# Kernel tuning notes

Measured on AMD Instinct MI355X. Metric: run time of the kernel, lower is better.

Reference implementation:

```python
import jax, jax.numpy as jnp
import numpy as np

WINDOW_SIZE = 11
NUM_BINS = 256
SIGMA = 1.5
C1 = 0.01 ** 2
C2 = 0.03 ** 2
MAX_PSNR = 40.0


def _gaussian_window():
    xs = jnp.arange(WINDOW_SIZE, dtype=jnp.float32)
    g = jnp.exp(-((xs - WINDOW_SIZE // 2) ** 2) / (2.0 * SIGMA ** 2))
    g = g / g.sum()
    w2 = jnp.outer(g, g)  # [11,11]
    return jnp.broadcast_to(w2[None, None], (3, 1, WINDOW_SIZE, WINDOW_SIZE))


def setup_inputs() -> dict:
    key = jax.random.key(0)
    k1, k2 = jax.random.split(key)
    B, C, H, W = 64, 3, 256, 256
    x = jax.random.uniform(k1, (B, C, H, W), dtype=jnp.float32) * 2.0 - 1.0
    y = jax.random.uniform(k2, (B, C, H, W), dtype=jnp.float32) * 2.0 - 1.0
    return {"x": x, "y": y, "window": _gaussian_window()}


def _depthwise_conv(img, w):
    pad = WINDOW_SIZE // 2
    return jax.lax.conv_general_dilated(
        img, w, window_strides=(1, 1), padding=[(pad, pad), (pad, pad)],
        feature_group_count=img.shape[1],
        dimension_numbers=("NCHW", "OIHW", "NCHW"))


def _mi(x, y):
    B = x.shape[0]
    nb = NUM_BINS
    xf = (x.reshape(B, -1) + 1.0) * 0.5  # [B, N] in [0,1]
    yf = (y.reshape(B, -1) + 1.0) * 0.5
    N = xf.shape[1]
    ix = jnp.clip((xf * nb).astype(jnp.int32), 0, nb - 1)
    iy = jnp.clip((yf * nb).astype(jnp.int32), 0, nb - 1)
    flat = (jnp.arange(B, dtype=jnp.int32)[:, None] * (nb * nb) + ix * nb + iy).reshape(-1)
    hist = jnp.zeros(B * nb * nb, jnp.float32).at[flat].add(1.0).reshape(B, nb, nb)
    jp = hist / N  # joint probs [B, nb, nb]
    px = jp.sum(axis=2)  # [B, nb]
    py = jp.sum(axis=1)

    def ent(p):
        return -jnp.sum(jnp.where(p > 0, p * jnp.log2(jnp.where(p > 0, p, 1.0)), 0.0), axis=-1)

    hx = ent(px)
    hy = ent(py)
    pxy = px[:, :, None] * py[:, None, :]
    ratio = jp / jnp.where(pxy > 0, pxy, 1.0)
    mi = jnp.sum(jnp.where(jp > 0, jp * jnp.log2(jnp.where(jp > 0, ratio, 1.0)), 0.0), axis=(1, 2))
    norm = jnp.minimum(hx, hy)  # mi_method='min'
    mi = jnp.where(norm > 0, mi / norm, 0.0)
    return jnp.clip(mi, 0.0, 1.0)


def _ssim(x, y, window):
    mu1 = _depthwise_conv(x, window)
    mu2 = _depthwise_conv(y, window)
    mu1_sq = mu1 * mu1
    mu2_sq = mu2 * mu2
    mu1_mu2 = mu1 * mu2
    sigma1_sq = _depthwise_conv(x * x, window) - mu1_sq
    sigma2_sq = _depthwise_conv(y * y, window) - mu2_sq
    sigma12 = _depthwise_conv(x * y, window) - mu1_mu2
    ssim_map = ((2 * mu1_mu2 + C1) * (2 * sigma12 + C2)) / ((mu1_sq + mu2_sq + C1) * (sigma1_sq + sigma2_sq + C2))
    return ssim_map.mean(axis=(1, 2, 3))


def _psnr(x, y):
    xr = x * 0.5 + 0.5
    yr = y * 0.5 + 0.5
    mse = jnp.mean((xr - yr) ** 2, axis=(1, 2, 3))
    zero = mse == 0
    mse = jnp.where(zero, 1e-8, mse)
    psnr = -10.0 * jnp.log10(mse)  # 20*log10(1.0) == 0
    return jnp.where(zero, 100.0, psnr) / MAX_PSNR


def reference(x, y, window):
    mi_vals = _mi(x, y)
    ssim_vals = _ssim(x, y, window)
    psnr_vals = _psnr(x, y)
    metrics = jnp.stack([mi_vals, ssim_vals, psnr_vals], axis=1)  # [B,3]
    return metrics[:, :, None]  # [B,3,1]
```

## Files before the change

### kernel.cpp

```cpp
#include <hip/hip_runtime.h>
#include <cstdint>
#include <cstddef>

#define BATCH 64
#define CH 3
#define HH 256
#define WW 256
#define NBINS 256
#define TILE 32
#define HALO 5
#define NPB (CH*HH*WW)
#define QPX (NPB/4)
#define NHB 256

__device__ __forceinline__ float block_reduce_256(float v, float* buf4) {
    #pragma unroll
    for (int o = 32; o > 0; o >>= 1) v += __shfl_down(v, o, 64);
    __syncthreads();
    int lane = threadIdx.x & 63;
    int wid  = threadIdx.x >> 6;
    if (lane == 0) buf4[wid] = v;
    __syncthreads();
    return buf4[0] + buf4[1] + buf4[2] + buf4[3];
}

__device__ __forceinline__ float block_reduce_1024(float v, float* buf16) {
    #pragma unroll
    for (int o = 32; o > 0; o >>= 1) v += __shfl_down(v, o, 64);
    __syncthreads();
    int lane = threadIdx.x & 63;
    int wid  = threadIdx.x >> 6;
    if (lane == 0) buf16[wid] = v;
    __syncthreads();
    float s = 0.0f;
    #pragma unroll
    for (int i = 0; i < 16; i++) s += buf16[i];
    return s;
}

__global__ __launch_bounds__(256) void mega_kernel(
    const float* __restrict__ x, const float* __restrict__ y,
    const float* __restrict__ win,
    float* __restrict__ ssim_partials,
    unsigned int* __restrict__ u4hist, float* __restrict__ mse_part)
{
    __shared__ __align__(16) unsigned char smem[32768];
    const int bid = blockIdx.x;
    const int tid = threadIdx.x;

    if (bid < NHB) {
        unsigned int* h32 = (unsigned int*)smem;
        uint4* h128 = (uint4*)h32;
        #pragma unroll
        for (int i = 0; i < 8; i++) h128[tid + i * 256] = make_uint4(0, 0, 0, 0);
        __syncthreads();

        const int b = bid >> 2, e = bid & 3;
        const float4* x4 = (const float4*)x + (size_t)b * (NPB/4) + (size_t)e * (QPX/4);
        const float4* y4 = (const float4*)y + (size_t)b * (NPB/4) + (size_t)e * (QPX/4);
        float mse_s = 0.0f;
        for (int i = 0; i < 48; i++) {
            float4 xv = x4[tid + i * 256];
            float4 yv = y4[tid + i * 256];
            float xs[4] = {xv.x, xv.y, xv.z, xv.w};
            float ys[4] = {yv.x, yv.y, yv.z, yv.w};
            #pragma unroll
            for (int q = 0; q < 4; q++) {
                float xc = xs[q], yc = ys[q];
                float d = xc - yc;
                mse_s += d * d;
                int ix = (int)(((xc + 1.0f) * 0.5f) * 256.0f);
                int iy = (int)(((yc + 1.0f) * 0.5f) * 256.0f);
                ix = min(max(ix, 0), 255);
                iy = min(max(iy, 0), 255);
                int key = ix * NBINS + iy;
                atomicAdd(&h32[key >> 3], 1u << (4 * (key & 7)));
            }
        }
        #pragma unroll
        for (int o = 32; o > 0; o >>= 1) mse_s += __shfl_down(mse_s, o, 64);
        if ((tid & 63) == 0) mse_part[bid * 4 + (tid >> 6)] = mse_s;
        __syncthreads();

        #pragma unroll
        for (int k = 0; k < 32; k++)
            u4hist[(size_t)bid * 8192 + tid + k * 256] = h32[tid + k * 256];
        return;
    }

    typedef float4 (*hA4_t)[33];
    hA4_t hA4 = (hA4_t)smem;
    float* g    = (float*)(smem + 22176);
    float* rbuf = (float*)(smem + 22240);

    const int cb = bid - NHB;
    const int tx = cb & 7, ty = (cb >> 3) & 7, z = cb >> 6;
    const float* xi = x + (size_t)z * (HH * WW);
    const float* yi = y + (size_t)z * (HH * WW);

    if (tid < 11) {
        float g5 = sqrtf(win[5*11 + 5]);
        g[tid] = win[5*11 + tid] / g5;
    }
    __syncthreads();

    if (tid < 42 * 4) {
        int r = tid >> 2;
        int c0 = (tid & 3) * 8;
        int gr = ty * TILE - HALO + r;
        int gw = tx * TILE + c0 - HALO;
        float xw[18], yw[18];
        bool rowok = (gr >= 0 && gr < HH);
        if (rowok) {
            const float* xr = xi + gr * WW;
            const float* yr = yi + gr * WW;
            int ga = gw - 3;
            if (ga >= 0 && ga + 24 <= WW) {
                float t0[24], t1[24];
                const float4* px4 = (const float4*)(xr + ga);
                const float4* py4 = (const float4*)(yr + ga);
                #pragma unroll
                for (int q = 0; q < 6; q++) {
                    float4 a = px4[q], bb = py4[q];
                    t0[q*4+0]=a.x; t0[q*4+1]=a.y; t0[q*4+2]=a.z; t0[q*4+3]=a.w;
                    t1[q*4+0]=bb.x; t1[q*4+1]=bb.y; t1[q*4+2]=bb.z; t1[q*4+3]=bb.w;
                }
                #pragma unroll
                for (int i = 0; i < 18; i++) { xw[i] = t0[3+i]; yw[i] = t1[3+i]; }
            } else {
                #pragma unroll
                for (int i = 0; i < 18; i++) {
                    int gc = gw + i;
                    bool ok = (gc >= 0 && gc < WW);
                    xw[i] = ok ? xr[gc] : 0.0f;
                    yw[i] = ok ? yr[gc] : 0.0f;
                }
            }
        } else {
            #pragma unroll
            for (int i = 0; i < 18; i++) { xw[i] = 0.0f; yw[i] = 0.0f; }
        }

        float aX[8], aY[8], aU[8], aV[8];
        #pragma unroll
        for (int j = 0; j < 8; j++) { aX[j]=0; aY[j]=0; aU[j]=0; aV[j]=0; }
        #pragma unroll
        for (int i = 0; i < 18; i++) {
            float xv = xw[i], yv = yw[i];
            float uu = xv * xv + yv * yv;
            float vv = xv * yv;
            #pragma unroll
            for (int j = 0; j < 8; j++) {
                int k = i - j;
                if (k >= 0 && k < 11) {
                    float w = g[k];
                    aX[j] += w * xv;
                    aY[j] += w * yv;
                    aU[j] += w * uu;
                    aV[j] += w * vv;
                }
            }
        }
        #pragma unroll
        for (int j = 0; j < 8; j++)
            hA4[r][c0 + j] = make_float4(aX[j], aY[j], aU[j], aV[j]);
    }
    __syncthreads();

    const int c  = tid & 31;
    const int r0 = (tid >> 5) * 4;
    float mu1[4], mu2[4], euv[4], exy[4];
    #pragma unroll
    for (int j = 0; j < 4; j++) { mu1[j]=0; mu2[j]=0; euv[j]=0; exy[j]=0; }
    #pragma unroll
    for (int i = 0; i < 14; i++) {
        float4 v = hA4[r0 + i][c];
        #pragma unroll
        for (int j = 0; j < 4; j++) {
            int k = i - j;
            if (k >= 0 && k < 11) {
                float w = g[k];
                mu1[j] += w * v.x;
                mu2[j] += w * v.y;
                euv[j] += w * v.z;
                exy[j] += w * v.w;
            }
        }
    }

    float ssim_s = 0.0f;
    const float C1v = 1e-4f, C2v = 9e-4f;
    #pragma unroll
    for (int j = 0; j < 4; j++) {
        float m1 = mu1[j], m2 = mu2[j];
        float m1s = m1 * m1, m2s = m2 * m2, m12 = m1 * m2;
        float ssum = euv[j] - m1s - m2s;
        float s12  = exy[j] - m12;
        float num = (2.0f * m12 + C1v) * (2.0f * s12 + C2v);
        float den = (m1s + m2s + C1v) * (ssum + C2v);
        ssim_s += num / den;
    }

    float ssim_b = block_reduce_256(ssim_s, rbuf);
    if (tid == 0)
        ssim_partials[(size_t)z * 64 + ty * 8 + tx] = ssim_b;
}

__global__ __launch_bounds__(1024) void merge_finalize_kernel(
    const unsigned int* __restrict__ u4hist,
    const float* __restrict__ mse_part, const float* __restrict__ ssim_partials,
    float* __restrict__ out)
{
    __shared__ unsigned int colw[16][256];
    __shared__ float rbuf[16];
    const int b = blockIdx.x, t = threadIdx.x;
    const int w = t >> 6, l = t & 63;
    const float invN = 1.0f / (float)NPB;

    #pragma unroll
    for (int i = 0; i < 4; i++) ((unsigned int*)colw)[t + i * 1024] = 0;
    __syncthreads();

    float sxy = 0.0f, sx = 0.0f;
    for (int s = 0; s < 4; s++) {
        unsigned int s0a = 0, s1a = 0, s0b = 0, s1b = 0;
        #pragma unroll
        for (int p = 0; p < 4; p++) {
            const uint2* src = (const uint2*)(u4hist + (size_t)(b * 4 + p) * 8192 + s * 2048);
            uint2 v = src[t];
            s0a += v.x & 0x0F0F0F0Fu;  s1a += (v.x >> 4) & 0x0F0F0F0Fu;
            s0b += v.y & 0x0F0F0F0Fu;  s1b += (v.y >> 4) & 0x0F0F0F0Fu;
        }
        unsigned int cnt[16];
        #pragma unroll
        for (int m = 0; m < 4; m++) {
            cnt[2*m]         = (s0a >> (8*m)) & 255u;
            cnt[2*m + 1]     = (s1a >> (8*m)) & 255u;
            cnt[8 + 2*m]     = (s0b >> (8*m)) & 255u;
            cnt[8 + 2*m + 1] = (s1b >> (8*m)) & 255u;
        }

        unsigned int rowc = 0;
        #pragma unroll
        for (int k = 0; k < 16; k++) {
            unsigned int v = cnt[k];
            rowc += v;
            if (v) {
                float jp = (float)v * invN;
                sxy += jp * __log2f(jp);
            }
        }
        #pragma unroll
        for (int o = 8; o > 0; o >>= 1) rowc += __shfl_xor((int)rowc, o, 16);
        if ((t & 15) == 0 && rowc) {
            float px = (float)rowc * invN;
            sx += px * __log2f(px);
        }

        #pragma unroll
        for (int k = 0; k < 16; k++) {
            cnt[k] += __shfl_xor((int)cnt[k], 16, 64);
            cnt[k] += __shfl_xor((int)cnt[k], 32, 64);
        }
        if (l < 16) {
            #pragma unroll
            for (int k = 0; k < 16; k++) colw[w][16 * l + k] += cnt[k];
        }
    }

    float sxy_blk = block_reduce_1024(sxy, rbuf);
    float sx_blk  = block_reduce_1024(sx, rbuf);

    float ey = 0.0f;
    if (t < 256) {
        unsigned int pc = 0;
        #pragma unroll
        for (int ww = 0; ww < 16; ww++) pc += colw[ww][t];
        if (pc) {
            float py = (float)pc * invN;
            ey = -py * __log2f(py);
        }
    }
    float hy = block_reduce_1024(ey, rbuf);
    float ssim_total = block_reduce_1024(
        (t < 192) ? ssim_partials[(size_t)b * 192 + t] : 0.0f, rbuf);
    float mse_all = block_reduce_1024(
        (t < 16) ? mse_part[b * 16 + t] : 0.0f, rbuf);

    if (t == 0) {
        float hxy = -sxy_blk;
        float hx  = -sx_blk;
        float mi = hx + hy - hxy;
        float norm = fminf(hx, hy);
        float m = (norm > 0.0f) ? (mi / norm) : 0.0f;
        m = fminf(fmaxf(m, 0.0f), 1.0f);
        out[b * 3 + 0] = m;
        out[b * 3 + 1] = ssim_total * invN;
        double mse = (double)mse_all * (1.0 / (4.0 * (double)NPB));
        out[b * 3 + 2] = (mse == 0.0) ? 2.5f : (float)(-10.0 * log10(mse) / 40.0);
    }
}

extern "C" void kernel_launch(void* const* d_in, const int* in_sizes, int n_in,
                              void* d_out, int out_size, void* d_ws, size_t ws_size,
                              hipStream_t stream) {
    const float* x   = (const float*)d_in[0];
    const float* y   = (const float*)d_in[1];
    const float* win = (const float*)d_in[2];
    float* out = (float*)d_out;

    char* p = (char*)d_ws;
    unsigned int* u4hist = (unsigned int*)p;
    size_t off = (size_t)NHB * 8192 * sizeof(unsigned int);
    float* mse_part = (float*)(p + off);        off += (size_t)NHB * 4 * sizeof(float);
    float* ssim_partials = (float*)(p + off);

    mega_kernel<<<dim3(NHB + 8 * 8 * BATCH * CH), dim3(256), 0, stream>>>(
        x, y, win, ssim_partials, u4hist, mse_part);
    merge_finalize_kernel<<<dim3(BATCH), dim3(1024), 0, stream>>>(
        u4hist, mse_part, ssim_partials, out);
}
```

Measured before the change: 183.7 us.

## Replace 2D tiled SSIM with per-column streaming row sweep over bands

The SSIM blocks now each own one 32-row band of a full 256-wide image plane. Each thread owns one column and sweeps 42 rows. A row is double-buffered through per-wave shared memory, the horizontal 11-tap pass is computed per row, and the vertical pass uses an 11-deep register sliding accumulator. This cuts halo recomputation from 2D tiles and removes the large shared tile plus its block-wide barriers, and it lowers the SSIM block count. The cost is a serial 42-iteration loop per thread with scalar loads, a heavier register footprint under the new launch-bounds occupancy hint, fewer blocks for the GPU to schedule, and a fast approximate divide.

```diff
diff --git a/kernel.cpp b/kernel.cpp
--- a/kernel.cpp
+++ b/kernel.cpp
@@ -7,11 +7,12 @@
 #define HH 256
 #define WW 256
 #define NBINS 256
-#define TILE 32
-#define HALO 5
 #define NPB (CH*HH*WW)
 #define QPX (NPB/4)
 #define NHB 256
+#define NZ (BATCH*CH)
+#define NBANDS 8
+#define NCB (NZ*NBANDS)
 
 __device__ __forceinline__ float block_reduce_256(float v, float* buf4) {
     #pragma unroll
@@ -38,7 +39,7 @@
     return s;
 }
 
-__global__ __launch_bounds__(256) void mega_kernel(
+__global__ __launch_bounds__(256, 5) void mega_kernel(
     const float* __restrict__ x, const float* __restrict__ y,
     const float* __restrict__ win,
     float* __restrict__ ssim_partials,
@@ -88,122 +89,114 @@
         return;
     }
 
-    typedef float4 (*hA4_t)[33];
-    hA4_t hA4 = (hA4_t)smem;
-    float* g    = (float*)(smem + 22176);
-    float* rbuf = (float*)(smem + 22240);
+    float* wbuf = (float*)smem;
+    float* rbuf = (float*)(smem + 5120);
 
     const int cb = bid - NHB;
-    const int tx = cb & 7, ty = (cb >> 3) & 7, z = cb >> 6;
+    const int z = cb >> 3, band = cb & 7;
+    const int w = tid >> 6, l = tid & 63;
+    float* wb = wbuf + w * 320;
+
     const float* xi = x + (size_t)z * (HH * WW);
     const float* yi = y + (size_t)z * (HH * WW);
 
-    if (tid < 11) {
-        float g5 = sqrtf(win[5*11 + 5]);
-        g[tid] = win[5*11 + tid] / g5;
-    }
-    __syncthreads();
-
-    if (tid < 42 * 4) {
-        int r = tid >> 2;
-        int c0 = (tid & 3) * 8;
-        int gr = ty * TILE - HALO + r;
-        int gw = tx * TILE + c0 - HALO;
-        float xw[18], yw[18];
-        bool rowok = (gr >= 0 && gr < HH);
-        if (rowok) {
+    float gw[11];
+    {
+        float gs = sqrtf(win[60]);
+        #pragma unroll
+        for (int k = 0; k < 11; k++) gw[k] = win[55 + k] / gs;
+    }
+
+    const int r0g = band * 32 - 5;
+    const int gc  = tid - 5;
+    const int gc2 = gc + 64;
+    const bool okc  = (gc >= 0);
+    const bool okc2 = (gc2 < WW);
+
+    float aX[11], aY[11], aU[11], aV[11];
+    #pragma unroll
+    for (int j = 0; j < 11; j++) { aX[j]=0.0f; aY[j]=0.0f; aU[j]=0.0f; aV[j]=0.0f; }
+
+    {
+        int gr = r0g;
+        bool okr = (gr >= 0) && (gr < HH);
+        const float* xr = xi + gr * WW;
+        const float* yr = yi + gr * WW;
+        float xv = (okr && okc) ? xr[gc] : 0.0f;
+        float yv = (okr && okc) ? yr[gc] : 0.0f;
+        wb[l]      = xv;
+        wb[80 + l] = yv;
+        if (l < 10) {
+            float xv2 = (okr && okc2) ? xr[gc2] : 0.0f;
+            float yv2 = (okr && okc2) ? yr[gc2] : 0.0f;
+            wb[l + 64]      = xv2;
+            wb[80 + l + 64] = yv2;
+        }
+    }
+
+    float ssim_s = 0.0f;
+    const float C1v = 1e-4f, C2v = 9e-4f;
+    #pragma unroll 1
+    for (int r = 0; r < 42; ++r) {
+        const int p = r & 1;
+        float* cur = wb + p * 160;
+        if (r < 41) {
+            int gr = r0g + r + 1;
+            bool okr = (gr >= 0) && (gr < HH);
             const float* xr = xi + gr * WW;
             const float* yr = yi + gr * WW;
-            int ga = gw - 3;
-            if (ga >= 0 && ga + 24 <= WW) {
-                float t0[24], t1[24];
-                const float4* px4 = (const float4*)(xr + ga);
-                const float4* py4 = (const float4*)(yr + ga);
-                #pragma unroll
-                for (int q = 0; q < 6; q++) {
-                    float4 a = px4[q], bb = py4[q];
-                    t0[q*4+0]=a.x; t0[q*4+1]=a.y; t0[q*4+2]=a.z; t0[q*4+3]=a.w;
-                    t1[q*4+0]=bb.x; t1[q*4+1]=bb.y; t1[q*4+2]=bb.z; t1[q*4+3]=bb.w;
-                }
-                #pragma unroll
-                for (int i = 0; i < 18; i++) { xw[i] = t0[3+i]; yw[i] = t1[3+i]; }
-            } else {
-                #pragma unroll
-                for (int i = 0; i < 18; i++) {
-                    int gc = gw + i;
-                    bool ok = (gc >= 0 && gc < WW);
-                    xw[i] = ok ? xr[gc] : 0.0f;
-                    yw[i] = ok ? yr[gc] : 0.0f;
-                }
+            float xv = (okr && okc) ? xr[gc] : 0.0f;
+            float yv = (okr && okc) ? yr[gc] : 0.0f;
+            float* nxt = wb + (p ^ 1) * 160;
+            nxt[l]      = xv;
+            nxt[80 + l] = yv;
+            if (l < 10) {
+                float xv2 = (okr && okc2) ? xr[gc2] : 0.0f;
+                float yv2 = (okr && okc2) ? yr[gc2] : 0.0f;
+                nxt[l + 64]      = xv2;
+                nxt[80 + l + 64] = yv2;
             }
-        } else {
-            #pragma unroll
-            for (int i = 0; i < 18; i++) { xw[i] = 0.0f; yw[i] = 0.0f; }
-        }
-
-        float aX[8], aY[8], aU[8], aV[8];
-        #pragma unroll
-        for (int j = 0; j < 8; j++) { aX[j]=0; aY[j]=0; aU[j]=0; aV[j]=0; }
-        #pragma unroll
-        for (int i = 0; i < 18; i++) {
-            float xv = xw[i], yv = yw[i];
-            float uu = xv * xv + yv * yv;
-            float vv = xv * yv;
-            #pragma unroll
-            for (int j = 0; j < 8; j++) {
-                int k = i - j;
-                if (k >= 0 && k < 11) {
-                    float w = g[k];
-                    aX[j] += w * xv;
-                    aY[j] += w * yv;
-                    aU[j] += w * uu;
-                    aV[j] += w * vv;
-                }
-            }
-        }
-        #pragma unroll
-        for (int j = 0; j < 8; j++)
-            hA4[r][c0 + j] = make_float4(aX[j], aY[j], aU[j], aV[j]);
-    }
-    __syncthreads();
-
-    const int c  = tid & 31;
-    const int r0 = (tid >> 5) * 4;
-    float mu1[4], mu2[4], euv[4], exy[4];
-    #pragma unroll
-    for (int j = 0; j < 4; j++) { mu1[j]=0; mu2[j]=0; euv[j]=0; exy[j]=0; }
-    #pragma unroll
-    for (int i = 0; i < 14; i++) {
-        float4 v = hA4[r0 + i][c];
-        #pragma unroll
-        for (int j = 0; j < 4; j++) {
-            int k = i - j;
-            if (k >= 0 && k < 11) {
-                float w = g[k];
-                mu1[j] += w * v.x;
-                mu2[j] += w * v.y;
-                euv[j] += w * v.z;
-                exy[j] += w * v.w;
-            }
-        }
-    }
-
-    float ssim_s = 0.0f;
-    const float C1v = 1e-4f, C2v = 9e-4f;
-    #pragma unroll
-    for (int j = 0; j < 4; j++) {
-        float m1 = mu1[j], m2 = mu2[j];
-        float m1s = m1 * m1, m2s = m2 * m2, m12 = m1 * m2;
-        float ssum = euv[j] - m1s - m2s;
-        float s12  = exy[j] - m12;
-        float num = (2.0f * m12 + C1v) * (2.0f * s12 + C2v);
-        float den = (m1s + m2s + C1v) * (ssum + C2v);
-        ssim_s += num / den;
+        }
+        float hx = 0.0f, hy = 0.0f, hu = 0.0f, hv = 0.0f;
+        #pragma unroll
+        for (int k = 0; k < 11; ++k) {
+            float a  = cur[l + k];
+            float b2 = cur[80 + l + k];
+            float wk = gw[k];
+            hx = fmaf(wk, a, hx);
+            hy = fmaf(wk, b2, hy);
+            float uu = fmaf(b2, b2, a * a);
+            hu = fmaf(wk, uu, hu);
+            float vv = a * b2;
+            hv = fmaf(wk, vv, hv);
+        }
+        #pragma unroll
+        for (int j = 0; j < 11; ++j) {
+            float wj = gw[10 - j];
+            aX[j] = fmaf(wj, hx, aX[j]);
+            aY[j] = fmaf(wj, hy, aY[j]);
+            aU[j] = fmaf(wj, hu, aU[j]);
+            aV[j] = fmaf(wj, hv, aV[j]);
+        }
+        if (r >= 10) {
+            float m1 = aX[0], m2 = aY[0];
+            float m1s = m1 * m1, m2s = m2 * m2, m12 = m1 * m2;
+            float ssum = aU[0] - m1s - m2s;
+            float s12  = aV[0] - m12;
+            float num = (2.0f * m12 + C1v) * (2.0f * s12 + C2v);
+            float den = (m1s + m2s + C1v) * (ssum + C2v);
+            ssim_s += __fdividef(num, den);
+        }
+        #pragma unroll
+        for (int j = 0; j < 10; ++j) {
+            aX[j] = aX[j+1]; aY[j] = aY[j+1]; aU[j] = aU[j+1]; aV[j] = aV[j+1];
+        }
+        aX[10] = 0.0f; aY[10] = 0.0f; aU[10] = 0.0f; aV[10] = 0.0f;
     }
 
     float ssim_b = block_reduce_256(ssim_s, rbuf);
     if (tid == 0)
-        ssim_partials[(size_t)z * 64 + ty * 8 + tx] = ssim_b;
+        ssim_partials[(size_t)z * NBANDS + band] = ssim_b;
 }
 
 __global__ __launch_bounds__(1024) void merge_finalize_kernel(
@@ -283,7 +276,7 @@
     }
     float hy = block_reduce_1024(ey, rbuf);
     float ssim_total = block_reduce_1024(
-        (t < 192) ? ssim_partials[(size_t)b * 192 + t] : 0.0f, rbuf);
+        (t < 24) ? ssim_partials[(size_t)b * 24 + t] : 0.0f, rbuf);
     float mse_all = block_reduce_1024(
         (t < 16) ? mse_part[b * 16 + t] : 0.0f, rbuf);
 
@@ -315,7 +308,7 @@
     float* mse_part = (float*)(p + off);        off += (size_t)NHB * 4 * sizeof(float);
     float* ssim_partials = (float*)(p + off);
 
-    mega_kernel<<<dim3(NHB + 8 * 8 * BATCH * CH), dim3(256), 0, stream>>>(
+    mega_kernel<<<dim3(NHB + NCB), dim3(256), 0, stream>>>(
         x, y, win, ssim_partials, u4hist, mse_part);
     merge_finalize_kernel<<<dim3(BATCH), dim3(1024), 0, stream>>>(
         u4hist, mse_part, ssim_partials, out);
```

After: 422.2 us. +129.9%, slower.
